# Optimization experiments

Hardware: AMD Instinct MI355X
Metric: run time of the kernel (lower is better)

The kernel has to match this reference:

```python
import jax, jax.numpy as jnp
import numpy as np

N = 50000      # nodes
E = 1600000    # edges (avg degree 32)
R = 8          # relation types
G = 64         # graphs in batch
D_IN = 128
HID = 128
CLS = 10


def setup_inputs() -> dict:
    key = jax.random.key(0)
    ks = jax.random.split(key, 12)
    s = 0.05  # weight init scale
    return {
        "x": jax.random.normal(ks[0], (N, D_IN), dtype=jnp.float32),
        "edge_index": jax.random.randint(ks[1], (2, E), 0, N, dtype=jnp.int32),
        "edge_type": jax.random.randint(ks[2], (E,), 0, R, dtype=jnp.int32),
        "batch": jnp.sort(jax.random.randint(ks[3], (N,), 0, G, dtype=jnp.int32)),
        "W1": jax.random.normal(ks[4], (R, D_IN, HID), dtype=jnp.float32) * s,
        "root1": jax.random.normal(ks[5], (D_IN, HID), dtype=jnp.float32) * s,
        "b1": jax.random.normal(ks[6], (HID,), dtype=jnp.float32) * s,
        "W2": jax.random.normal(ks[7], (R, HID, HID), dtype=jnp.float32) * s,
        "root2": jax.random.normal(ks[8], (HID, HID), dtype=jnp.float32) * s,
        "b2": jax.random.normal(ks[9], (HID,), dtype=jnp.float32) * s,
        "lin_w": jax.random.normal(ks[10], (HID, CLS), dtype=jnp.float32) * s,
        "lin_b": jax.random.normal(ks[11], (CLS,), dtype=jnp.float32) * s,
    }


def rgcn_conv(x, edge_index, edge_type, W, root, bias):
    # PyG RGCNConv (default aggr='mean'): per-relation mean of neighbor
    # features, relation-specific matmul, summed over relations, + root + bias.
    src, dst = edge_index[0], edge_index[1]
    d_in = x.shape[1]
    seg = dst * R + edge_type                      # fused (node, relation) segment id
    msg = jax.ops.segment_sum(x[src], seg, num_segments=N * R)          # [N*R, d_in]
    cnt = jax.ops.segment_sum(jnp.ones((E,), x.dtype), seg, num_segments=N * R)
    mean = (msg / jnp.maximum(cnt, 1.0)[:, None]).reshape(N, R, d_in)   # [N, R, d_in]
    return jnp.einsum('nrd,rdh->nh', mean, W) + x @ root + bias


def reference(x, edge_index, edge_type, batch, W1, root1, b1, W2, root2, b2, lin_w, lin_b):
    h = jax.nn.relu(rgcn_conv(x, edge_index, edge_type, W1, root1, b1))
    h = jax.nn.relu(rgcn_conv(h, edge_index, edge_type, W2, root2, b2))
    # global mean pool per graph
    gsum = jax.ops.segment_sum(h, batch, num_segments=G)                # [G, HID]
    gcnt = jax.ops.segment_sum(jnp.ones((N,), h.dtype), batch, num_segments=G)
    g = gsum / jnp.maximum(gcnt, 1.0)[:, None]
    return g @ lin_w + lin_b                                            # [G, CLS]
```

## Files before the change

kernel.cpp:

```cpp
#include <hip/hip_runtime.h>

#define N_NODES 50000
#define N_EDGES 1600000
#define R_REL 8
#define G_GRAPHS 64
#define D_INF 128
#define HIDF 128
#define CLSF 10

#define S_SEG (N_NODES * R_REL)
#define RZ 9
#define PCHUNK 16

#define XG 8
#define NODES_PER_G (N_NODES / XG)
#define SORT_BLKS_PER_G 256
#define SORT_GRID (XG * SORT_BLKS_PER_G)

typedef __attribute__((ext_vector_type(8))) short short8;
typedef __attribute__((ext_vector_type(4))) float floatx4;

typedef __attribute__((address_space(1))) const unsigned int guint;
typedef __attribute__((address_space(3))) unsigned int luint;
__device__ __forceinline__ void gload_lds16(const void* g, void* l) {
    __builtin_amdgcn_global_load_lds((guint*)g, (luint*)l, 16, 0, 0);
}

__device__ __forceinline__ unsigned short f2bf(float f) {
    unsigned int u = __float_as_uint(f);
    unsigned int r = (u + 0x7fffu + ((u >> 16) & 1u)) >> 16;
    return (unsigned short)r;
}
__device__ __forceinline__ float bflo(unsigned int u) { return __uint_as_float(u << 16); }
__device__ __forceinline__ float bfhi(unsigned int u) { return __uint_as_float(u & 0xffff0000u); }

__device__ __forceinline__ int ntload(const int* p) { return __builtin_nontemporal_load(p); }

__global__ __launch_bounds__(256) void seg_kernel(const int* __restrict__ dst,
                                                  const int* __restrict__ et,
                                                  int* __restrict__ seg) {
    int i4 = blockIdx.x * 256 + threadIdx.x;
    if (i4 * 4 >= N_EDGES) return;
    int4 d = ((const int4*)dst)[i4];
    int4 t = ((const int4*)et)[i4];
    int4 s;
    s.x = d.x * R_REL + t.x; s.y = d.y * R_REL + t.y;
    s.z = d.z * R_REL + t.z; s.w = d.w * R_REL + t.w;
    ((int4*)seg)[i4] = s;
}

__global__ __launch_bounds__(256) void count_kernel(const int* __restrict__ seg,
                                                    int* __restrict__ cnt) {
    int xg = blockIdx.x & (XG - 1);
    int inner = blockIdx.x >> 3;
    int lo = xg * NODES_PER_G * R_REL, hi = lo + NODES_PER_G * R_REL;
    for (int e = inner * 256 + threadIdx.x; e < N_EDGES; e += SORT_BLKS_PER_G * 256) {
        int sg = ntload(seg + e);
        if (sg >= lo && sg < hi) atomicAdd(&cnt[sg], 1);
    }
}

#define SCAN_BLK 256
#define SCAN_ELEMS 1024
#define NB_SCAN ((S_SEG + SCAN_ELEMS - 1) / SCAN_ELEMS)

__global__ __launch_bounds__(SCAN_BLK) void scan1_kernel(const int* __restrict__ cnt,
                                                         int* __restrict__ off,
                                                         int* __restrict__ bsum) {
    __shared__ int sd[SCAN_BLK];
    int t = threadIdx.x;
    int base = blockIdx.x * SCAN_ELEMS + t * 4;
    int v[4];
    int tsum = 0;
#pragma unroll
    for (int j = 0; j < 4; j++) {
        v[j] = (base + j < S_SEG) ? cnt[base + j] : 0;
        tsum += v[j];
    }
    sd[t] = tsum;
    __syncthreads();
    for (int d = 1; d < SCAN_BLK; d <<= 1) {
        int x = (t >= d) ? sd[t - d] : 0;
        __syncthreads();
        sd[t] += x;
        __syncthreads();
    }
    int incl = sd[t];
    int run = incl - tsum;
#pragma unroll
    for (int j = 0; j < 4; j++) {
        if (base + j < S_SEG) off[base + j] = run;
        run += v[j];
    }
    if (t == SCAN_BLK - 1) bsum[blockIdx.x] = incl;
}

__global__ __launch_bounds__(512) void absoff2_kernel(int* __restrict__ off,
                                                      const int* __restrict__ bsum,
                                                      int* __restrict__ cursor) {
    __shared__ int sd[512];
    int t = threadIdx.x;
    int v = (t < NB_SCAN) ? bsum[t] : 0;
    sd[t] = v;
    __syncthreads();
    for (int d = 1; d < 512; d <<= 1) {
        int x = (t >= d) ? sd[t - d] : 0;
        __syncthreads();
        sd[t] += x;
        __syncthreads();
    }
    int pre = (blockIdx.x == 0) ? 0 : sd[blockIdx.x - 1];
    int base = blockIdx.x * SCAN_ELEMS + t * 2;
#pragma unroll
    for (int j = 0; j < 2; j++) {
        int i = base + j;
        if (i < S_SEG) {
            int o = off[i] + pre;
            off[i] = o;
            cursor[i] = o;
        }
    }
}

__global__ __launch_bounds__(256) void bin_kernel(const int* __restrict__ seg,
                                                  const int* __restrict__ src,
                                                  int* __restrict__ cursor,
                                                  unsigned short* __restrict__ esrc) {
    int xg = blockIdx.x & (XG - 1);
    int inner = blockIdx.x >> 3;
    int lo = xg * NODES_PER_G * R_REL, hi = lo + NODES_PER_G * R_REL;
    for (int e = inner * 256 + threadIdx.x; e < N_EDGES; e += SORT_BLKS_PER_G * 256) {
        int sg = ntload(seg + e);
        if (sg >= lo && sg < hi) {
            int pos = atomicAdd(&cursor[sg], 1);
            esrc[pos] = (unsigned short)ntload(src + e);
        }
    }
}

__global__ void convx_kernel(const float* __restrict__ x, unsigned short* __restrict__ xb) {
    int idx = blockIdx.x * blockDim.x + threadIdx.x;
    if (idx < N_NODES * D_INF) xb[idx] = f2bf(x[idx]);
}

__global__ __launch_bounds__(256) void convw9_kernel(const float* __restrict__ W,
                                                     const float* __restrict__ root,
                                                     unsigned short* __restrict__ wz) {
    __shared__ float t[16][17];
    int r = blockIdx.z;
    int k0 = blockIdx.x * 16, c0 = blockIdx.y * 16;
    int tx = threadIdx.x & 15, ty = threadIdx.x >> 4;
    const float* srcp = (r < 8) ? (W + (size_t)r * 128 * 128) : root;
    t[ty][tx] = srcp[(size_t)(k0 + ty) * 128 + c0 + tx];
    __syncthreads();
    wz[(size_t)r * 16384 + (size_t)(c0 + ty) * 128 + k0 + tx] = f2bf(t[tx][ty]);
}

__global__ __launch_bounds__(256) void agg_mean(
    const unsigned short* __restrict__ hsrc,
    const unsigned short* __restrict__ esrc,
    const int* __restrict__ off,
    unsigned short* __restrict__ m)
{
    int sg = blockIdx.x * 16 + (threadIdx.x >> 4);
    int l = threadIdx.x & 15;
    int beg = off[sg];
    int end = (sg + 1 < S_SEG) ? off[sg + 1] : N_EDGES;
    float w = 1.0f / (float)max(end - beg, 1);

    float a0 = 0.f, a1 = 0.f, a2 = 0.f, a3 = 0.f;
    float a4 = 0.f, a5 = 0.f, a6 = 0.f, a7 = 0.f;
    int e = beg;
    for (; e + 4 <= end; e += 4) {
        int s0 = esrc[e], s1 = esrc[e + 1], s2 = esrc[e + 2], s3 = esrc[e + 3];
        uint4 v0 = *(const uint4*)(hsrc + (size_t)s0 * HIDF + l * 8);
        uint4 v1 = *(const uint4*)(hsrc + (size_t)s1 * HIDF + l * 8);
        uint4 v2 = *(const uint4*)(hsrc + (size_t)s2 * HIDF + l * 8);
        uint4 v3 = *(const uint4*)(hsrc + (size_t)s3 * HIDF + l * 8);
        a0 += bflo(v0.x) + bflo(v1.x) + bflo(v2.x) + bflo(v3.x);
        a1 += bfhi(v0.x) + bfhi(v1.x) + bfhi(v2.x) + bfhi(v3.x);
        a2 += bflo(v0.y) + bflo(v1.y) + bflo(v2.y) + bflo(v3.y);
        a3 += bfhi(v0.y) + bfhi(v1.y) + bfhi(v2.y) + bfhi(v3.y);
        a4 += bflo(v0.z) + bflo(v1.z) + bflo(v2.z) + bflo(v3.z);
        a5 += bfhi(v0.z) + bfhi(v1.z) + bfhi(v2.z) + bfhi(v3.z);
        a6 += bflo(v0.w) + bflo(v1.w) + bflo(v2.w) + bflo(v3.w);
        a7 += bfhi(v0.w) + bfhi(v1.w) + bfhi(v2.w) + bfhi(v3.w);
    }
    for (; e < end; e++) {
        int s0 = esrc[e];
        uint4 v0 = *(const uint4*)(hsrc + (size_t)s0 * HIDF + l * 8);
        a0 += bflo(v0.x); a1 += bfhi(v0.x);
        a2 += bflo(v0.y); a3 += bfhi(v0.y);
        a4 += bflo(v0.z); a5 += bfhi(v0.z);
        a6 += bflo(v0.w); a7 += bfhi(v0.w);
    }
    uint4 o;
    o.x = (unsigned int)f2bf(a0 * w) | ((unsigned int)f2bf(a1 * w) << 16);
    o.y = (unsigned int)f2bf(a2 * w) | ((unsigned int)f2bf(a3 * w) << 16);
    o.z = (unsigned int)f2bf(a4 * w) | ((unsigned int)f2bf(a5 * w) << 16);
    o.w = (unsigned int)f2bf(a6 * w) | ((unsigned int)f2bf(a7 * w) << 16);
    *(uint4*)(m + (size_t)sg * HIDF + l * 8) = o;
}

__global__ __launch_bounds__(256) void transform9(
    const unsigned short* __restrict__ mm,
    const unsigned short* __restrict__ hsrc,
    const unsigned short* __restrict__ wz,
    const float* __restrict__ bias,
    unsigned short* __restrict__ hout)
{
    __shared__ __align__(16) unsigned short A4[4][128][32];
    __shared__ __align__(16) unsigned short B4[4][128][32];

    const int tx = threadIdx.x;
    const int wave = tx >> 6, lane = tx & 63;
    const int quad = lane >> 4, lq = lane & 15;
    const int srow = lane >> 2, sch = lane & 3;
    const int row0 = blockIdx.x * 128;

    floatx4 acc[2][8];
#pragma unroll
    for (int i = 0; i < 2; i++)
#pragma unroll
        for (int j = 0; j < 8; j++) acc[i][j] = (floatx4){0.f, 0.f, 0.f, 0.f};

    for (int r = 0; r < RZ; r++) {
#pragma unroll
        for (int kk = 0; kk < 4; kk++) {
#pragma unroll
            for (int p = 0; p < 2; p++) {
                int rr = (wave * 2 + p) * 16;
                int gr = row0 + rr + srow; if (gr >= N_NODES) gr = N_NODES - 1;
                const unsigned short* ap = (r < 8)
                    ? mm + (size_t)gr * (R_REL * HIDF) + r * HIDF
                    : hsrc + (size_t)gr * HIDF;
                gload_lds16(ap + kk * 32 + sch * 8, &A4[kk][rr][0]);
                gload_lds16(wz + ((size_t)r * 128 + rr + srow) * 128 + kk * 32 + sch * 8,
                            &B4[kk][rr][0]);
            }
        }
        __syncthreads();

#pragma unroll
        for (int kk = 0; kk < 4; kk++) {
            short8 af[2], bfr[8];
#pragma unroll
            for (int i = 0; i < 2; i++)
                af[i] = *(const short8*)(&A4[kk][wave * 32 + i * 16 + lq][quad * 8]);
#pragma unroll
            for (int j = 0; j < 8; j++)
                bfr[j] = *(const short8*)(&B4[kk][j * 16 + lq][quad * 8]);
#pragma unroll
            for (int i = 0; i < 2; i++)
#pragma unroll
                for (int j = 0; j < 8; j++)
                    acc[i][j] = __builtin_amdgcn_mfma_f32_16x16x32_bf16(af[i], bfr[j], acc[i][j], 0, 0, 0);
        }
        __syncthreads();
    }

#pragma unroll
    for (int i = 0; i < 2; i++)
#pragma unroll
        for (int j = 0; j < 8; j++) {
            int col = j * 16 + lq;
            float bv = bias[col];
#pragma unroll
            for (int rg = 0; rg < 4; rg++) {
                int row = row0 + wave * 32 + i * 16 + quad * 4 + rg;
                if (row < N_NODES)
                    hout[(size_t)row * HIDF + col] = f2bf(fmaxf(acc[i][j][rg] + bv, 0.f));
            }
        }
}

__global__ __launch_bounds__(256) void pool1_kernel(const unsigned short* __restrict__ h,
                                                    const int* __restrict__ batch,
                                                    float* __restrict__ partial) {
    int g = blockIdx.x;
    int p = blockIdx.y;
    int lo, hi;
    {
        int l = 0, r = N_NODES;
        while (l < r) { int m = (l + r) >> 1; if (batch[m] < g) l = m + 1; else r = m; }
        lo = l;
        l = lo; r = N_NODES;
        while (l < r) { int m = (l + r) >> 1; if (batch[m] < g + 1) l = m + 1; else r = m; }
        hi = l;
    }
    int t = threadIdx.x;
    int rowlane = t >> 5;
    int c4 = t & 31;
    float a0 = 0.f, a1 = 0.f, a2 = 0.f, a3 = 0.f;
    for (int n = lo + p + rowlane * PCHUNK; n < hi; n += 8 * PCHUNK) {
        uint2 v = *(const uint2*)(h + (size_t)n * HIDF + c4 * 4);
        a0 += bflo(v.x); a1 += bfhi(v.x); a2 += bflo(v.y); a3 += bfhi(v.y);
    }
    __shared__ float red[8][128];
    if (rowlane == 0) {
        red[0][c4 * 4 + 0] = a0; red[0][c4 * 4 + 1] = a1;
        red[0][c4 * 4 + 2] = a2; red[0][c4 * 4 + 3] = a3;
    }
    __syncthreads();
    for (int s = 1; s < 8; s++) {
        if (rowlane == s) {
            red[0][c4 * 4 + 0] += a0; red[0][c4 * 4 + 1] += a1;
            red[0][c4 * 4 + 2] += a2; red[0][c4 * 4 + 3] += a3;
        }
        __syncthreads();
    }
    if (t < 128) partial[((size_t)g * PCHUNK + p) * 128 + t] = red[0][t];
}

__global__ __launch_bounds__(128) void poolfin_kernel(const float* __restrict__ partial,
                                                      const int* __restrict__ batch,
                                                      const float* __restrict__ lin_w,
                                                      const float* __restrict__ lin_b,
                                                      float* __restrict__ out) {
    __shared__ float gl[HIDF];
    int g = blockIdx.x;
    int lo, hi;
    {
        int l = 0, r = N_NODES;
        while (l < r) { int m = (l + r) >> 1; if (batch[m] < g) l = m + 1; else r = m; }
        lo = l;
        l = lo; r = N_NODES;
        while (l < r) { int m = (l + r) >> 1; if (batch[m] < g + 1) l = m + 1; else r = m; }
        hi = l;
    }
    int t = threadIdx.x;
    float s = 0.f;
#pragma unroll
    for (int p = 0; p < PCHUNK; p++)
        s += partial[((size_t)g * PCHUNK + p) * 128 + t];
    gl[t] = s / (float)max(hi - lo, 1);
    __syncthreads();
    if (t < CLSF) {
        float acc = lin_b[t];
#pragma unroll 16
        for (int d = 0; d < HIDF; d++) acc += gl[d] * lin_w[d * CLSF + t];
        out[g * CLSF + t] = acc;
    }
}

extern "C" void kernel_launch(void* const* d_in, const int* in_sizes, int n_in,
                              void* d_out, int out_size, void* d_ws, size_t ws_size,
                              hipStream_t stream) {
    const float* x     = (const float*)d_in[0];
    const int*   ei    = (const int*)d_in[1];
    const int*   et    = (const int*)d_in[2];
    const int*   batch = (const int*)d_in[3];
    const float* W1    = (const float*)d_in[4];
    const float* root1 = (const float*)d_in[5];
    const float* b1    = (const float*)d_in[6];
    const float* W2    = (const float*)d_in[7];
    const float* root2 = (const float*)d_in[8];
    const float* b2    = (const float*)d_in[9];
    const float* lin_w = (const float*)d_in[10];
    const float* lin_b = (const float*)d_in[11];
    float* out = (float*)d_out;

    const int* src = ei;
    const int* dst = ei + N_EDGES;

    char* ws = (char*)d_ws;
    unsigned short* xb  = (unsigned short*)ws; ws += (size_t)N_NODES * HIDF * 2;
    unsigned short* h1  = (unsigned short*)ws; ws += (size_t)N_NODES * HIDF * 2;
    unsigned short* h2  = (unsigned short*)ws; ws += (size_t)N_NODES * HIDF * 2;
    unsigned short* m   = (unsigned short*)ws; ws += (size_t)S_SEG * HIDF * 2;
    unsigned short* wz1 = (unsigned short*)ws; ws += (size_t)RZ * 128 * 128 * 2;
    unsigned short* wz2 = (unsigned short*)ws; ws += (size_t)RZ * 128 * 128 * 2;
    int*   seg    = (int*)ws;   ws += (size_t)N_EDGES * 4;
    int*   cnt    = (int*)ws;   ws += (size_t)S_SEG * 4;
    int*   off    = (int*)ws;   ws += (size_t)S_SEG * 4;
    int*   bsum   = (int*)ws;   ws += 512 * 4;
    int*   cursor = (int*)ws;   ws += (size_t)S_SEG * 4;
    unsigned short* esrc = (unsigned short*)ws; ws += (size_t)N_EDGES * 2;
    float* partial = (float*)ws; ws += (size_t)G_GRAPHS * PCHUNK * 128 * 4;

    hipMemsetAsync(cnt, 0, (size_t)S_SEG * 4, stream);

    seg_kernel<<<(N_EDGES / 4 + 255) / 256, 256, 0, stream>>>(dst, et, seg);
    count_kernel<<<SORT_GRID, 256, 0, stream>>>(seg, cnt);
    scan1_kernel<<<NB_SCAN, SCAN_BLK, 0, stream>>>(cnt, off, bsum);
    absoff2_kernel<<<NB_SCAN, 512, 0, stream>>>(off, bsum, cursor);
    bin_kernel<<<SORT_GRID, 256, 0, stream>>>(seg, src, cursor, esrc);

    convx_kernel<<<(N_NODES * D_INF + 255) / 256, 256, 0, stream>>>(x, xb);
    convw9_kernel<<<dim3(8, 8, RZ), 256, 0, stream>>>(W1, root1, wz1);
    convw9_kernel<<<dim3(8, 8, RZ), 256, 0, stream>>>(W2, root2, wz2);

    const int NGB = (N_NODES + 127) / 128;
    const int NSB = S_SEG / 16;

    agg_mean<<<NSB, 256, 0, stream>>>(xb, esrc, off, m);
    transform9<<<NGB, 256, 0, stream>>>(m, xb, wz1, b1, h1);

    agg_mean<<<NSB, 256, 0, stream>>>(h1, esrc, off, m);
    transform9<<<NGB, 256, 0, stream>>>(m, h1, wz2, b2, h2);

    pool1_kernel<<<dim3(G_GRAPHS, PCHUNK), 256, 0, stream>>>(h2, batch, partial);
    poolfin_kernel<<<G_GRAPHS, 128, 0, stream>>>(partial, batch, lin_w, lin_b, out);

    (void)in_sizes; (void)n_in; (void)out_size; (void)ws_size;
}
```

Baseline: 461.7 us.

## Fuse relation mean aggregation with relation-weight MFMA transform per node tile

Merges the agg_mean and transform9 kernels into one fused_layer kernel. Each block aggregates 8 relation means for 16 nodes into LDS, then runs the 9 MFMA GEMMs directly from LDS, so the large bf16 intermediate m (N*R*128) is never written to or read back from global memory. The cost is that every block reloads the full 9x128x128 weight set for only 16 rows, so weight traffic per output row grows about eightfold. MFMA work per wave also shrinks to 2 tiles, lowering compute density.

```diff
diff --git a/kernel.cpp b/kernel.cpp
--- a/kernel.cpp
+++ b/kernel.cpp
@@ -156,122 +156,108 @@
     wz[(size_t)r * 16384 + (size_t)(c0 + ty) * 128 + k0 + tx] = f2bf(t[tx][ty]);
 }
 
-__global__ __launch_bounds__(256) void agg_mean(
+__global__ __launch_bounds__(256) void fused_layer(
     const unsigned short* __restrict__ hsrc,
     const unsigned short* __restrict__ esrc,
     const int* __restrict__ off,
-    unsigned short* __restrict__ m)
-{
-    int sg = blockIdx.x * 16 + (threadIdx.x >> 4);
-    int l = threadIdx.x & 15;
-    int beg = off[sg];
-    int end = (sg + 1 < S_SEG) ? off[sg + 1] : N_EDGES;
-    float w = 1.0f / (float)max(end - beg, 1);
-
-    float a0 = 0.f, a1 = 0.f, a2 = 0.f, a3 = 0.f;
-    float a4 = 0.f, a5 = 0.f, a6 = 0.f, a7 = 0.f;
-    int e = beg;
-    for (; e + 4 <= end; e += 4) {
-        int s0 = esrc[e], s1 = esrc[e + 1], s2 = esrc[e + 2], s3 = esrc[e + 3];
-        uint4 v0 = *(const uint4*)(hsrc + (size_t)s0 * HIDF + l * 8);
-        uint4 v1 = *(const uint4*)(hsrc + (size_t)s1 * HIDF + l * 8);
-        uint4 v2 = *(const uint4*)(hsrc + (size_t)s2 * HIDF + l * 8);
-        uint4 v3 = *(const uint4*)(hsrc + (size_t)s3 * HIDF + l * 8);
-        a0 += bflo(v0.x) + bflo(v1.x) + bflo(v2.x) + bflo(v3.x);
-        a1 += bfhi(v0.x) + bfhi(v1.x) + bfhi(v2.x) + bfhi(v3.x);
-        a2 += bflo(v0.y) + bflo(v1.y) + bflo(v2.y) + bflo(v3.y);
-        a3 += bfhi(v0.y) + bfhi(v1.y) + bfhi(v2.y) + bfhi(v3.y);
-        a4 += bflo(v0.z) + bflo(v1.z) + bflo(v2.z) + bflo(v3.z);
-        a5 += bfhi(v0.z) + bfhi(v1.z) + bfhi(v2.z) + bfhi(v3.z);
-        a6 += bflo(v0.w) + bflo(v1.w) + bflo(v2.w) + bflo(v3.w);
-        a7 += bfhi(v0.w) + bfhi(v1.w) + bfhi(v2.w) + bfhi(v3.w);
-    }
-    for (; e < end; e++) {
-        int s0 = esrc[e];
-        uint4 v0 = *(const uint4*)(hsrc + (size_t)s0 * HIDF + l * 8);
-        a0 += bflo(v0.x); a1 += bfhi(v0.x);
-        a2 += bflo(v0.y); a3 += bfhi(v0.y);
-        a4 += bflo(v0.z); a5 += bfhi(v0.z);
-        a6 += bflo(v0.w); a7 += bfhi(v0.w);
-    }
-    uint4 o;
-    o.x = (unsigned int)f2bf(a0 * w) | ((unsigned int)f2bf(a1 * w) << 16);
-    o.y = (unsigned int)f2bf(a2 * w) | ((unsigned int)f2bf(a3 * w) << 16);
-    o.z = (unsigned int)f2bf(a4 * w) | ((unsigned int)f2bf(a5 * w) << 16);
-    o.w = (unsigned int)f2bf(a6 * w) | ((unsigned int)f2bf(a7 * w) << 16);
-    *(uint4*)(m + (size_t)sg * HIDF + l * 8) = o;
-}
-
-__global__ __launch_bounds__(256) void transform9(
-    const unsigned short* __restrict__ mm,
-    const unsigned short* __restrict__ hsrc,
     const unsigned short* __restrict__ wz,
     const float* __restrict__ bias,
     unsigned short* __restrict__ hout)
 {
-    __shared__ __align__(16) unsigned short A4[4][128][32];
+    __shared__ __align__(16) unsigned short A8[8][4][16][32];
     __shared__ __align__(16) unsigned short B4[4][128][32];
 
     const int tx = threadIdx.x;
     const int wave = tx >> 6, lane = tx & 63;
     const int quad = lane >> 4, lq = lane & 15;
     const int srow = lane >> 2, sch = lane & 3;
-    const int row0 = blockIdx.x * 128;
-
-    floatx4 acc[2][8];
-#pragma unroll
-    for (int i = 0; i < 2; i++)
-#pragma unroll
-        for (int j = 0; j < 8; j++) acc[i][j] = (floatx4){0.f, 0.f, 0.f, 0.f};
+    const int n0 = blockIdx.x * 16;
+    const int grp = tx >> 4;
+    const int l = tx & 15;
+
+    const int node = n0 + grp;
+#pragma unroll 1
+    for (int r = 0; r < R_REL; r++) {
+        int sg = node * R_REL + r;
+        int beg = off[sg];
+        int end = (sg + 1 < S_SEG) ? off[sg + 1] : N_EDGES;
+        float w = 1.0f / (float)max(end - beg, 1);
+        float a0 = 0.f, a1 = 0.f, a2 = 0.f, a3 = 0.f;
+        float a4 = 0.f, a5 = 0.f, a6 = 0.f, a7 = 0.f;
+        int e = beg;
+        for (; e + 4 <= end; e += 4) {
+            int s0 = esrc[e], s1 = esrc[e + 1], s2 = esrc[e + 2], s3 = esrc[e + 3];
+            uint4 v0 = *(const uint4*)(hsrc + (size_t)s0 * HIDF + l * 8);
+            uint4 v1 = *(const uint4*)(hsrc + (size_t)s1 * HIDF + l * 8);
+            uint4 v2 = *(const uint4*)(hsrc + (size_t)s2 * HIDF + l * 8);
+            uint4 v3 = *(const uint4*)(hsrc + (size_t)s3 * HIDF + l * 8);
+            a0 += bflo(v0.x) + bflo(v1.x) + bflo(v2.x) + bflo(v3.x);
+            a1 += bfhi(v0.x) + bfhi(v1.x) + bfhi(v2.x) + bfhi(v3.x);
+            a2 += bflo(v0.y) + bflo(v1.y) + bflo(v2.y) + bflo(v3.y);
+            a3 += bfhi(v0.y) + bfhi(v1.y) + bfhi(v2.y) + bfhi(v3.y);
+            a4 += bflo(v0.z) + bflo(v1.z) + bflo(v2.z) + bflo(v3.z);
+            a5 += bfhi(v0.z) + bfhi(v1.z) + bfhi(v2.z) + bfhi(v3.z);
+            a6 += bflo(v0.w) + bflo(v1.w) + bflo(v2.w) + bflo(v3.w);
+            a7 += bfhi(v0.w) + bfhi(v1.w) + bfhi(v2.w) + bfhi(v3.w);
+        }
+        for (; e < end; e++) {
+            int s0 = esrc[e];
+            uint4 v0 = *(const uint4*)(hsrc + (size_t)s0 * HIDF + l * 8);
+            a0 += bflo(v0.x); a1 += bfhi(v0.x);
+            a2 += bflo(v0.y); a3 += bfhi(v0.y);
+            a4 += bflo(v0.z); a5 += bfhi(v0.z);
+            a6 += bflo(v0.w); a7 += bfhi(v0.w);
+        }
+        uint4 o;
+        o.x = (unsigned int)f2bf(a0 * w) | ((unsigned int)f2bf(a1 * w) << 16);
+        o.y = (unsigned int)f2bf(a2 * w) | ((unsigned int)f2bf(a3 * w) << 16);
+        o.z = (unsigned int)f2bf(a4 * w) | ((unsigned int)f2bf(a5 * w) << 16);
+        o.w = (unsigned int)f2bf(a6 * w) | ((unsigned int)f2bf(a7 * w) << 16);
+        *(uint4*)&A8[r][l >> 2][grp][(l & 3) * 8] = o;
+    }
+
+    floatx4 acc[2];
+    acc[0] = (floatx4){0.f, 0.f, 0.f, 0.f};
+    acc[1] = (floatx4){0.f, 0.f, 0.f, 0.f};
 
     for (int r = 0; r < RZ; r++) {
 #pragma unroll
-        for (int kk = 0; kk < 4; kk++) {
+        for (int kk = 0; kk < 4; kk++)
 #pragma unroll
             for (int p = 0; p < 2; p++) {
                 int rr = (wave * 2 + p) * 16;
-                int gr = row0 + rr + srow; if (gr >= N_NODES) gr = N_NODES - 1;
-                const unsigned short* ap = (r < 8)
-                    ? mm + (size_t)gr * (R_REL * HIDF) + r * HIDF
-                    : hsrc + (size_t)gr * HIDF;
-                gload_lds16(ap + kk * 32 + sch * 8, &A4[kk][rr][0]);
                 gload_lds16(wz + ((size_t)r * 128 + rr + srow) * 128 + kk * 32 + sch * 8,
                             &B4[kk][rr][0]);
             }
-        }
         __syncthreads();
 
 #pragma unroll
         for (int kk = 0; kk < 4; kk++) {
-            short8 af[2], bfr[8];
-#pragma unroll
-            for (int i = 0; i < 2; i++)
-                af[i] = *(const short8*)(&A4[kk][wave * 32 + i * 16 + lq][quad * 8]);
-#pragma unroll
-            for (int j = 0; j < 8; j++)
-                bfr[j] = *(const short8*)(&B4[kk][j * 16 + lq][quad * 8]);
-#pragma unroll
-            for (int i = 0; i < 2; i++)
-#pragma unroll
-                for (int j = 0; j < 8; j++)
-                    acc[i][j] = __builtin_amdgcn_mfma_f32_16x16x32_bf16(af[i], bfr[j], acc[i][j], 0, 0, 0);
-        }
-        __syncthreads();
-    }
-
-#pragma unroll
-    for (int i = 0; i < 2; i++)
-#pragma unroll
-        for (int j = 0; j < 8; j++) {
-            int col = j * 16 + lq;
-            float bv = bias[col];
-#pragma unroll
-            for (int rg = 0; rg < 4; rg++) {
-                int row = row0 + wave * 32 + i * 16 + quad * 4 + rg;
-                if (row < N_NODES)
-                    hout[(size_t)row * HIDF + col] = f2bf(fmaxf(acc[i][j][rg] + bv, 0.f));
-            }
-        }
+            short8 af, bfr[2];
+            if (r < 8)
+                af = *(const short8*)(&A8[r][kk][lq][quad * 8]);
+            else
+                af = *(const short8*)(hsrc + (size_t)(n0 + lq) * HIDF + kk * 32 + quad * 8);
+#pragma unroll
+            for (int j = 0; j < 2; j++)
+                bfr[j] = *(const short8*)(&B4[kk][wave * 32 + j * 16 + lq][quad * 8]);
+#pragma unroll
+            for (int j = 0; j < 2; j++)
+                acc[j] = __builtin_amdgcn_mfma_f32_16x16x32_bf16(af, bfr[j], acc[j], 0, 0, 0);
+        }
+        __syncthreads();
+    }
+
+#pragma unroll
+    for (int j = 0; j < 2; j++) {
+        int col = wave * 32 + j * 16 + lq;
+        float bv = bias[col];
+#pragma unroll
+        for (int rg = 0; rg < 4; rg++) {
+            int row = n0 + quad * 4 + rg;
+            hout[(size_t)row * HIDF + col] = f2bf(fmaxf(acc[j][rg] + bv, 0.f));
+        }
+    }
 }
 
 __global__ __launch_bounds__(256) void pool1_kernel(const unsigned short* __restrict__ h,
@@ -367,7 +353,6 @@
     unsigned short* xb  = (unsigned short*)ws; ws += (size_t)N_NODES * HIDF * 2;
     unsigned short* h1  = (unsigned short*)ws; ws += (size_t)N_NODES * HIDF * 2;
     unsigned short* h2  = (unsigned short*)ws; ws += (size_t)N_NODES * HIDF * 2;
-    unsigned short* m   = (unsigned short*)ws; ws += (size_t)S_SEG * HIDF * 2;
     unsigned short* wz1 = (unsigned short*)ws; ws += (size_t)RZ * 128 * 128 * 2;
     unsigned short* wz2 = (unsigned short*)ws; ws += (size_t)RZ * 128 * 128 * 2;
     int*   seg    = (int*)ws;   ws += (size_t)N_EDGES * 4;
@@ -390,14 +375,10 @@
     convw9_kernel<<<dim3(8, 8, RZ), 256, 0, stream>>>(W1, root1, wz1);
     convw9_kernel<<<dim3(8, 8, RZ), 256, 0, stream>>>(W2, root2, wz2);
 
-    const int NGB = (N_NODES + 127) / 128;
-    const int NSB = S_SEG / 16;
-
-    agg_mean<<<NSB, 256, 0, stream>>>(xb, esrc, off, m);
-    transform9<<<NGB, 256, 0, stream>>>(m, xb, wz1, b1, h1);
-
-    agg_mean<<<NSB, 256, 0, stream>>>(h1, esrc, off, m);
-    transform9<<<NGB, 256, 0, stream>>>(m, h1, wz2, b2, h2);
+    const int NFB = N_NODES / 16;
+
+    fused_layer<<<NFB, 256, 0, stream>>>(xb, esrc, off, wz1, b1, h1);
+    fused_layer<<<NFB, 256, 0, stream>>>(h1, esrc, off, wz2, b2, h2);
 
     pool1_kernel<<<dim3(G_GRAPHS, PCHUNK), 256, 0, stream>>>(h2, batch, partial);
     poolfin_kernel<<<G_GRAPHS, 128, 0, stream>>>(partial, batch, lin_w, lin_b, out);
```

New measurement: 678.7 us. 47.0% more time.
